# Optimization experiments

Hardware: AMD Instinct MI355X
Metric: run time of the kernel (lower is better)

## Reference

```python
import jax, jax.numpy as jnp
import numpy as np

SPATIAL_SHAPES = [(128, 128), (64, 64), (32, 32), (16, 16)]  # (H_l, W_l) per level
NUM_HEADS = 8
NUM_LEVELS = 4
NUM_POINTS = 4
EMBED_DIM = 256
HEAD_DIM = EMBED_DIM // NUM_HEADS
LEN_V = sum(h * w for h, w in SPATIAL_SHAPES)  # 21760
BS, LQ = 8, 900


def setup_inputs() -> dict:
    key = jax.random.key(0)
    ks = jax.random.split(key, 12)
    s = 0.05
    return {
        'query': jax.random.normal(ks[0], (BS, LQ, EMBED_DIM), jnp.float32),
        'reference_points': jax.random.uniform(ks[1], (BS, LQ, NUM_LEVELS, 2), jnp.float32),
        'value': jax.random.normal(ks[2], (BS, LEN_V, EMBED_DIM), jnp.float32),
        'w_value': jax.random.normal(ks[3], (EMBED_DIM, EMBED_DIM), jnp.float32) * s,
        'b_value': jnp.zeros((EMBED_DIM,), jnp.float32),
        'w_off': jax.random.normal(ks[4], (EMBED_DIM, NUM_HEADS * NUM_LEVELS * NUM_POINTS * 2), jnp.float32) * s,
        'b_off': jax.random.normal(ks[5], (NUM_HEADS * NUM_LEVELS * NUM_POINTS * 2,), jnp.float32),
        'w_attn': jax.random.normal(ks[6], (EMBED_DIM, NUM_HEADS * NUM_LEVELS * NUM_POINTS), jnp.float32) * s,
        'b_attn': jnp.zeros((NUM_HEADS * NUM_LEVELS * NUM_POINTS,), jnp.float32),
        'w_out': jax.random.normal(ks[7], (EMBED_DIM, EMBED_DIM), jnp.float32) * s,
        'b_out': jnp.zeros((EMBED_DIM,), jnp.float32),
    }


def _bilinear_sample(val, locx, locy, H, W):
    # val: [bs, nh, H*W, hd]; locx/locy: [bs, nh, N] normalized in [0,1]
    # grid_sample semantics: align_corners=False, zero padding.
    px = locx * W - 0.5
    py = locy * H - 0.5
    x0 = jnp.floor(px)
    y0 = jnp.floor(py)
    dx = px - x0
    dy = py - y0
    x0i = x0.astype(jnp.int32)
    y0i = y0.astype(jnp.int32)
    out = jnp.zeros(val.shape[:2] + (locx.shape[-1], val.shape[-1]), val.dtype)
    corners = [
        (x0i, y0i, (1 - dx) * (1 - dy)),
        (x0i + 1, y0i, dx * (1 - dy)),
        (x0i, y0i + 1, (1 - dx) * dy),
        (x0i + 1, y0i + 1, dx * dy),
    ]
    for xi, yi, w in corners:
        valid = ((xi >= 0) & (xi < W) & (yi >= 0) & (yi < H)).astype(val.dtype)
        idx = jnp.clip(yi, 0, H - 1) * W + jnp.clip(xi, 0, W - 1)
        g = jnp.take_along_axis(val, idx[..., None], axis=2)  # [bs,nh,N,hd]
        out = out + g * (w * valid)[..., None]
    return out


def reference(query, reference_points, value, w_value, b_value, w_off, b_off,
              w_attn, b_attn, w_out, b_out):
    bs, Lq, C = query.shape
    # value projection -> [bs, Lv, nh, hd]
    v = (value @ w_value + b_value).reshape(bs, -1, NUM_HEADS, HEAD_DIM)
    # sampling offsets [bs,Lq,nh,L,P,2], attention weights softmax over L*P
    off = (query @ w_off + b_off).reshape(bs, Lq, NUM_HEADS, NUM_LEVELS, NUM_POINTS, 2)
    aw = (query @ w_attn + b_attn).reshape(bs, Lq, NUM_HEADS, NUM_LEVELS * NUM_POINTS)
    aw = jax.nn.softmax(aw, axis=-1).reshape(bs, Lq, NUM_HEADS, NUM_LEVELS, NUM_POINTS)
    # normalizer is (W_l, H_l) per level (flip of spatial shapes)
    norm = jnp.asarray([[w, h] for h, w in SPATIAL_SHAPES], query.dtype)  # [L,2]
    loc = reference_points[:, :, None, :, None, :] + off / norm[None, None, None, :, None, :]
    # per-level bilinear sampling and weighted reduction
    out = jnp.zeros((bs, Lq, NUM_HEADS, HEAD_DIM), query.dtype)
    start = 0
    for l, (H, W) in enumerate(SPATIAL_SHAPES):
        vl = v[:, start:start + H * W]                       # [bs,HW,nh,hd]
        vl = vl.transpose(0, 2, 1, 3)                        # [bs,nh,HW,hd]
        ll = loc[:, :, :, l].transpose(0, 2, 1, 3, 4)        # [bs,nh,Lq,P,2]
        ll = ll.reshape(bs, NUM_HEADS, Lq * NUM_POINTS, 2)
        s = _bilinear_sample(vl, ll[..., 0], ll[..., 1], H, W)
        s = s.reshape(bs, NUM_HEADS, Lq, NUM_POINTS, HEAD_DIM)
        out = out + jnp.einsum('bhqpd,bqhp->bqhd', s, aw[:, :, :, l])
        start += H * W
    out = out.reshape(bs, Lq, C)
    return out @ w_out + b_out
```

## Files before the change

kernel.cpp:

```cpp
#include <hip/hip_runtime.h>

#define BS 8
#define LQ 900
#define NH 8
#define NL 4
#define NP 4
#define HD 32
#define ED 256
#define LEN_V 21760

typedef __attribute__((ext_vector_type(8))) short bf16x8;
typedef __attribute__((ext_vector_type(4))) float f32x4;
typedef __attribute__((ext_vector_type(4))) float fv4;

static __device__ __forceinline__ unsigned short f2bf(float f) {
  union { float f; unsigned u; } x; x.f = f;
  unsigned r = x.u + 0x7fffu + ((x.u >> 16) & 1u);
  return (unsigned short)(r >> 16);
}
static __device__ __forceinline__ float bf2f(unsigned short s) {
  union { unsigned u; float f; } x; x.u = ((unsigned)s) << 16;
  return x.f;
}
static __device__ __forceinline__ unsigned pack2(float a, float b) {
  return (unsigned)f2bf(a) | ((unsigned)f2bf(b) << 16);
}

__global__ __launch_bounds__(256, 3) void vproj_kernel(
    const float* __restrict__ value, const float* __restrict__ w,
    const float* __restrict__ bias, unsigned short* __restrict__ vout) {
  const int t = threadIdx.x;
  const int row0 = blockIdx.x * 64;
  const int wv = t >> 6;
  const int lane = t & 63;
  const int quad = lane >> 4;
  const int nn = lane & 15;

  __shared__ unsigned short a_lds[4 * 64 * 8];
  __shared__ unsigned short b_lds[4 * 256 * 8];

  f32x4 acc[4][4];
#pragma unroll
  for (int i = 0; i < 4; i++)
#pragma unroll
    for (int j = 0; j < 4; j++) acc[i][j] = (f32x4)(0.f);

  const int arow = t >> 2;
  const int akseg = t & 3;
  const int bkseg = wv;
  const int bn = lane;

  for (int k0 = 0; k0 < 256; k0 += 32) {
    __syncthreads();
    {
      const float* pa = &value[(row0 + arow) * 256 + k0 + akseg * 8];
      fv4 v0 = __builtin_nontemporal_load((const fv4*)pa);
      fv4 v1 = __builtin_nontemporal_load((const fv4*)(pa + 4));
      uint4 pk;
      pk.x = pack2(v0.x, v0.y);
      pk.y = pack2(v0.z, v0.w);
      pk.z = pack2(v1.x, v1.y);
      pk.w = pack2(v1.z, v1.w);
      *(uint4*)&a_lds[(akseg * 64 + arow) * 8] = pk;
    }
    {
      const float* pb = &w[(k0 + bkseg * 8) * 256 + bn];
#pragma unroll
      for (int c = 0; c < 4; c++) {
        float f[8];
#pragma unroll
        for (int j = 0; j < 8; j++) f[j] = pb[j * 256 + c * 64];
        uint4 pk;
        pk.x = pack2(f[0], f[1]);
        pk.y = pack2(f[2], f[3]);
        pk.z = pack2(f[4], f[5]);
        pk.w = pack2(f[6], f[7]);
        *(uint4*)&b_lds[(bkseg * 256 + c * 64 + bn) * 8] = pk;
      }
    }
    __syncthreads();

    bf16x8 af[4], bf[4];
#pragma unroll
    for (int rt = 0; rt < 4; rt++)
      af[rt] = *(const bf16x8*)&a_lds[(quad * 64 + rt * 16 + nn) * 8];
#pragma unroll
    for (int ct = 0; ct < 4; ct++)
      bf[ct] = *(const bf16x8*)&b_lds[(quad * 256 + wv * 64 + ct * 16 + nn) * 8];
#pragma unroll
    for (int rt = 0; rt < 4; rt++)
#pragma unroll
      for (int ct = 0; ct < 4; ct++)
        acc[rt][ct] = __builtin_amdgcn_mfma_f32_16x16x32_bf16(
            af[rt], bf[ct], acc[rt][ct], 0, 0, 0);
  }

#pragma unroll
  for (int ct = 0; ct < 4; ct++) {
    const int col = wv * 64 + ct * 16 + nn;
    const float bv = bias[col];
    const int h = col >> 5;
    const int d = col & 31;
#pragma unroll
    for (int rt = 0; rt < 4; rt++) {
      f32x4 f = acc[rt][ct];
#pragma unroll
      for (int reg = 0; reg < 4; reg++) {
        const int grow = row0 + rt * 16 + quad * 4 + reg;
        const int b = grow / LEN_V;
        const int s = grow - b * LEN_V;
        vout[((b * NH + h) * LEN_V + s) * HD + d] = f2bf(f[reg] + bv);
      }
    }
  }
}

__global__ __launch_bounds__(384, 2) void offattn_kernel(
    const float* __restrict__ query,
    const float* __restrict__ w_off, const float* __restrict__ b_off,
    const float* __restrict__ w_attn, const float* __restrict__ b_attn,
    float* __restrict__ OFF, float* __restrict__ LOG) {
  const int t = threadIdx.x;
  const int row0 = blockIdx.x * 32;
  const int rg = t / 96;
  const int c4 = t % 96;
  const int col = c4 * 4;
  const bool isOff = col < 256;
  const float* wbase = isOff ? (w_off + col) : (w_attn + (col - 256));
  const int wstride = isOff ? 256 : 128;
  const float* bb = isOff ? (b_off + col) : (b_attn + (col - 256));
  __shared__ float a_lds[32][8];

  float4 acc[8];
#pragma unroll
  for (int r = 0; r < 8; r++) acc[r] = make_float4(0.f, 0.f, 0.f, 0.f);

  for (int k0 = 0; k0 < 256; k0 += 8) {
    __syncthreads();
    if (t < 256) a_lds[t >> 3][t & 7] = query[(row0 + (t >> 3)) * 256 + k0 + (t & 7)];
    __syncthreads();
    float4 wr[8];
#pragma unroll
    for (int k = 0; k < 8; k++)
      wr[k] = *(const float4*)&wbase[(k0 + k) * wstride];
#pragma unroll
    for (int r = 0; r < 8; r++) {
      const float* ar = &a_lds[rg * 8 + r][0];
      float4 a0 = *(const float4*)&ar[0];
      float4 a1 = *(const float4*)&ar[4];
      float4 s = acc[r];
      s.x += a0.x*wr[0].x + a0.y*wr[1].x + a0.z*wr[2].x + a0.w*wr[3].x
           + a1.x*wr[4].x + a1.y*wr[5].x + a1.z*wr[6].x + a1.w*wr[7].x;
      s.y += a0.x*wr[0].y + a0.y*wr[1].y + a0.z*wr[2].y + a0.w*wr[3].y
           + a1.x*wr[4].y + a1.y*wr[5].y + a1.z*wr[6].y + a1.w*wr[7].y;
      s.z += a0.x*wr[0].z + a0.y*wr[1].z + a0.z*wr[2].z + a0.w*wr[3].z
           + a1.x*wr[4].z + a1.y*wr[5].z + a1.z*wr[6].z + a1.w*wr[7].z;
      s.w += a0.x*wr[0].w + a0.y*wr[1].w + a0.z*wr[2].w + a0.w*wr[3].w
           + a1.x*wr[4].w + a1.y*wr[5].w + a1.z*wr[6].w + a1.w*wr[7].w;
      acc[r] = s;
    }
  }

  const float4 bv = *(const float4*)bb;
#pragma unroll
  for (int r = 0; r < 8; r++) {
    const int grow = row0 + rg * 8 + r;
    float4 o = make_float4(acc[r].x + bv.x, acc[r].y + bv.y,
                           acc[r].z + bv.z, acc[r].w + bv.w);
    if (isOff) *(float4*)&OFF[grow * 256 + col] = o;
    else       *(float4*)&LOG[grow * 128 + (col - 256)] = o;
  }
}

__global__ __launch_bounds__(256, 4) void sample_kernel(
    const float* __restrict__ refp, const unsigned short* __restrict__ vp,
    const float* __restrict__ OFF, const float* __restrict__ LOG,
    float* __restrict__ RES) {
  const int t = threadIdx.x;
  const int b = blockIdx.x / (LQ / 4);
  const int q0 = (blockIdx.x % (LQ / 4)) * 4;

  __shared__ float off_lds[4][256];
  __shared__ float aw_lds[4][128];
  __shared__ float ref_lds[4][4][2];
  __shared__ int   soff[512][4];
  __shared__ float swt[512][4];

#pragma unroll
  for (int qi = 0; qi < 4; qi++)
    off_lds[qi][t] = OFF[(b * LQ + q0 + qi) * 256 + t];
  if (t < 128) {
#pragma unroll
    for (int qi = 0; qi < 4; qi++)
      aw_lds[qi][t] = LOG[(b * LQ + q0 + qi) * 128 + t];
  }
  if (t < 32) {
    const int qi = t >> 3, l = (t >> 1) & 3, xy = t & 1;
    ref_lds[qi][l][xy] = refp[((b * LQ + q0 + qi) * NL + l) * 2 + xy];
  }
  __syncthreads();

  if (t < 32) {
    const int qi = t >> 3, h = t & 7;
    float* a = &aw_lds[qi][h * 16];
    float m = a[0];
#pragma unroll
    for (int i = 1; i < 16; i++) m = fmaxf(m, a[i]);
    float e[16];
    float ssum = 0.f;
#pragma unroll
    for (int i = 0; i < 16; i++) { e[i] = __expf(a[i] - m); ssum += e[i]; }
    const float inv = 1.f / ssum;
#pragma unroll
    for (int i = 0; i < 16; i++) a[i] = e[i] * inv;
  }
  __syncthreads();

#pragma unroll
  for (int ss = 0; ss < 2; ss++) {
    const int sid = t + ss * 256;
    const int p = sid & 3, l = (sid >> 2) & 3, h = (sid >> 4) & 7, qi = sid >> 7;
    const int W = 128 >> l;
    const int base = (l == 0) ? 0 : ((l == 1) ? 16384 : ((l == 2) ? 20480 : 21504));
    const float Wf = (float)W;
    const float refx = ref_lds[qi][l][0];
    const float refy = ref_lds[qi][l][1];
    const float offx = off_lds[qi][h * 32 + l * 8 + p * 2 + 0];
    const float offy = off_lds[qi][h * 32 + l * 8 + p * 2 + 1];
    const float aw = aw_lds[qi][h * 16 + l * 4 + p];
    const float px = refx * Wf + offx - 0.5f;
    const float py = refy * Wf + offy - 0.5f;
    const float x0f = floorf(px), y0f = floorf(py);
    const float dx = px - x0f, dy = py - y0f;
    const int x0 = (int)x0f, y0 = (int)y0f;
    const int x1 = x0 + 1, y1 = y0 + 1;
    const float mx0 = (x0 >= 0 && x0 < W) ? 1.f : 0.f;
    const float mx1 = (x1 >= 0 && x1 < W) ? 1.f : 0.f;
    const float my0 = (y0 >= 0 && y0 < W) ? 1.f : 0.f;
    const float my1 = (y1 >= 0 && y1 < W) ? 1.f : 0.f;
    const int x0c = min(max(x0, 0), W - 1);
    const int x1c = min(max(x1, 0), W - 1);
    const int y0c = min(max(y0, 0), W - 1);
    const int y1c = min(max(y1, 0), W - 1);
    soff[sid][0] = (base + y0c * W + x0c) * 16;
    soff[sid][1] = (base + y0c * W + x1c) * 16;
    soff[sid][2] = (base + y1c * W + x0c) * 16;
    soff[sid][3] = (base + y1c * W + x1c) * 16;
    swt[sid][0] = (1.f - dx) * (1.f - dy) * mx0 * my0 * aw;
    swt[sid][1] = dx * (1.f - dy) * mx1 * my0 * aw;
    swt[sid][2] = (1.f - dx) * dy * mx0 * my1 * aw;
    swt[sid][3] = dx * dy * mx1 * my1 * aw;
  }
  __syncthreads();

  const int qsel = t >> 7;
  const int hh = (t >> 4) & 7;
  const int d2 = t & 15;
  const unsigned* vpu = (const unsigned*)vp + (size_t)(b * NH + hh) * (LEN_V * HD / 2);
#pragma unroll
  for (int j = 0; j < 2; j++) {
    const int qi = qsel * 2 + j;
    float r0 = 0.f, r1 = 0.f;
#pragma unroll
    for (int lp = 0; lp < 16; lp++) {
      const int sid = ((qi * 8 + hh) << 4) + lp;
      const int4 o = *(const int4*)&soff[sid][0];
      const float4 w = *(const float4*)&swt[sid][0];
      const unsigned u00 = vpu[o.x + d2];
      const unsigned u10 = vpu[o.y + d2];
      const unsigned u01 = vpu[o.z + d2];
      const unsigned u11 = vpu[o.w + d2];
      r0 += w.x * bf2f((unsigned short)(u00 & 0xffff))
          + w.y * bf2f((unsigned short)(u10 & 0xffff))
          + w.z * bf2f((unsigned short)(u01 & 0xffff))
          + w.w * bf2f((unsigned short)(u11 & 0xffff));
      r1 += w.x * bf2f((unsigned short)(u00 >> 16))
          + w.y * bf2f((unsigned short)(u10 >> 16))
          + w.z * bf2f((unsigned short)(u01 >> 16))
          + w.w * bf2f((unsigned short)(u11 >> 16));
    }
    float2 rr = make_float2(r0, r1);
    *(float2*)&RES[(b * LQ + q0 + qi) * 256 + hh * 32 + d2 * 2] = rr;
  }
}

__global__ __launch_bounds__(256, 2) void outproj_kernel(
    const float* __restrict__ RES, const float* __restrict__ w,
    const float* __restrict__ bias, float* __restrict__ out) {
  const int t = threadIdx.x;
  const int row0 = blockIdx.x * 32;
  const int rg = t >> 6;
  const int c0 = (t & 63) << 2;
  __shared__ float a_lds[32][8];

  float4 acc[8];
#pragma unroll
  for (int r = 0; r < 8; r++) acc[r] = make_float4(0.f, 0.f, 0.f, 0.f);

  const int lr = t >> 3;
  const int lk = t & 7;
  for (int k0 = 0; k0 < 256; k0 += 8) {
    __syncthreads();
    a_lds[lr][lk] = RES[(row0 + lr) * 256 + k0 + lk];
    __syncthreads();
    float4 wr[8];
#pragma unroll
    for (int k = 0; k < 8; k++)
      wr[k] = *(const float4*)&w[(k0 + k) * 256 + c0];
#pragma unroll
    for (int r = 0; r < 8; r++) {
      const float* ar = &a_lds[rg * 8 + r][0];
      float4 a0 = *(const float4*)&ar[0];
      float4 a1 = *(const float4*)&ar[4];
      float4 s = acc[r];
      s.x += a0.x*wr[0].x + a0.y*wr[1].x + a0.z*wr[2].x + a0.w*wr[3].x
           + a1.x*wr[4].x + a1.y*wr[5].x + a1.z*wr[6].x + a1.w*wr[7].x;
      s.y += a0.x*wr[0].y + a0.y*wr[1].y + a0.z*wr[2].y + a0.w*wr[3].y
           + a1.x*wr[4].y + a1.y*wr[5].y + a1.z*wr[6].y + a1.w*wr[7].y;
      s.z += a0.x*wr[0].z + a0.y*wr[1].z + a0.z*wr[2].z + a0.w*wr[3].z
           + a1.x*wr[4].z + a1.y*wr[5].z + a1.z*wr[6].z + a1.w*wr[7].z;
      s.w += a0.x*wr[0].w + a0.y*wr[1].w + a0.z*wr[2].w + a0.w*wr[3].w
           + a1.x*wr[4].w + a1.y*wr[5].w + a1.z*wr[6].w + a1.w*wr[7].w;
      acc[r] = s;
    }
  }

  const float4 bv = *(const float4*)&bias[c0];
#pragma unroll
  for (int r = 0; r < 8; r++) {
    const int grow = row0 + rg * 8 + r;
    float4 o = make_float4(acc[r].x + bv.x, acc[r].y + bv.y,
                           acc[r].z + bv.z, acc[r].w + bv.w);
    *(float4*)&out[grow * 256 + c0] = o;
  }
}

extern "C" void kernel_launch(void* const* d_in, const int* in_sizes, int n_in,
                              void* d_out, int out_size, void* d_ws, size_t ws_size,
                              hipStream_t stream) {
  (void)in_sizes; (void)n_in; (void)out_size; (void)ws_size;
  const float* query   = (const float*)d_in[0];
  const float* refp    = (const float*)d_in[1];
  const float* value   = (const float*)d_in[2];
  const float* w_value = (const float*)d_in[3];
  const float* b_value = (const float*)d_in[4];
  const float* w_off   = (const float*)d_in[5];
  const float* b_off   = (const float*)d_in[6];
  const float* w_attn  = (const float*)d_in[7];
  const float* b_attn  = (const float*)d_in[8];
  const float* w_out   = (const float*)d_in[9];
  const float* b_out   = (const float*)d_in[10];
  float* out = (float*)d_out;

  char* ws = (char*)d_ws;
  unsigned short* vp = (unsigned short*)ws;
  float* OFF = (float*)(ws + 89128960);
  float* LOG = (float*)(ws + 89128960 + 7372800);
  float* RES = (float*)(ws + 89128960 + 7372800 + 3686400);

  vproj_kernel<<<(BS * LEN_V) / 64, 256, 0, stream>>>(value, w_value, b_value, vp);
  offattn_kernel<<<(BS * LQ) / 32, 384, 0, stream>>>(query, w_off, b_off,
                                                     w_attn, b_attn, OFF, LOG);
  sample_kernel<<<BS * (LQ / 4), 256, 0, stream>>>(refp, vp, OFF, LOG, RES);
  outproj_kernel<<<(BS * LQ) / 32, 256, 0, stream>>>(RES, w_out, b_out, out);
}
```

Baseline: 443.1 us.

## Pre-convert value weights to bf16 and load MFMA fragments directly from global

Adds a small prep kernel that converts w_value to bf16 once, in the MFMA-swizzled layout. The value-projection GEMM then drops its LDS staging and barriers: each wave loads its A fragments straight from global memory and converts them in registers, and reads B fragments from the pre-packed buffer. This removes the repeated per-block fp32 weight conversion and the shared-memory round trips. In exchange, the A rows are loaded redundantly by each of the four waves and the launch count grows by one.

```diff
diff --git a/kernel.cpp b/kernel.cpp
--- a/kernel.cpp
+++ b/kernel.cpp
@@ -25,9 +25,35 @@
 static __device__ __forceinline__ unsigned pack2(float a, float b) {
   return (unsigned)f2bf(a) | ((unsigned)f2bf(b) << 16);
 }
+static __device__ __forceinline__ bf16x8 pack8(fv4 a, fv4 b) {
+  union { uint4 u; bf16x8 h; } x;
+  x.u.x = pack2(a.x, a.y);
+  x.u.y = pack2(a.z, a.w);
+  x.u.z = pack2(b.x, b.y);
+  x.u.w = pack2(b.z, b.w);
+  return x.h;
+}
+
+__global__ __launch_bounds__(256) void bprep_kernel(
+    const float* __restrict__ w, unsigned short* __restrict__ Bsw) {
+  const int id = blockIdx.x * 256 + threadIdx.x;
+  const int n = id & 255;
+  const int kseg = (id >> 8) & 3;
+  const int kc = id >> 10;
+  const float* src = &w[(kc * 32 + kseg * 8) * 256 + n];
+  float f[8];
+#pragma unroll
+  for (int j = 0; j < 8; j++) f[j] = src[j * 256];
+  uint4 pk;
+  pk.x = pack2(f[0], f[1]);
+  pk.y = pack2(f[2], f[3]);
+  pk.z = pack2(f[4], f[5]);
+  pk.w = pack2(f[6], f[7]);
+  *(uint4*)&Bsw[((kc * 4 + kseg) * 256 + n) * 8] = pk;
+}
 
 __global__ __launch_bounds__(256, 3) void vproj_kernel(
-    const float* __restrict__ value, const float* __restrict__ w,
+    const float* __restrict__ value, const unsigned short* __restrict__ Bsw,
     const float* __restrict__ bias, unsigned short* __restrict__ vout) {
   const int t = threadIdx.x;
   const int row0 = blockIdx.x * 64;
@@ -36,63 +62,34 @@
   const int quad = lane >> 4;
   const int nn = lane & 15;
 
-  __shared__ unsigned short a_lds[4 * 64 * 8];
-  __shared__ unsigned short b_lds[4 * 256 * 8];
-
   f32x4 acc[4][4];
 #pragma unroll
   for (int i = 0; i < 4; i++)
 #pragma unroll
     for (int j = 0; j < 4; j++) acc[i][j] = (f32x4)(0.f);
 
-  const int arow = t >> 2;
-  const int akseg = t & 3;
-  const int bkseg = wv;
-  const int bn = lane;
-
-  for (int k0 = 0; k0 < 256; k0 += 32) {
-    __syncthreads();
-    {
-      const float* pa = &value[(row0 + arow) * 256 + k0 + akseg * 8];
-      fv4 v0 = __builtin_nontemporal_load((const fv4*)pa);
-      fv4 v1 = __builtin_nontemporal_load((const fv4*)(pa + 4));
-      uint4 pk;
-      pk.x = pack2(v0.x, v0.y);
-      pk.y = pack2(v0.z, v0.w);
-      pk.z = pack2(v1.x, v1.y);
-      pk.w = pack2(v1.z, v1.w);
-      *(uint4*)&a_lds[(akseg * 64 + arow) * 8] = pk;
-    }
-    {
-      const float* pb = &w[(k0 + bkseg * 8) * 256 + bn];
-#pragma unroll
-      for (int c = 0; c < 4; c++) {
-        float f[8];
-#pragma unroll
-        for (int j = 0; j < 8; j++) f[j] = pb[j * 256 + c * 64];
-        uint4 pk;
-        pk.x = pack2(f[0], f[1]);
-        pk.y = pack2(f[2], f[3]);
-        pk.z = pack2(f[4], f[5]);
-        pk.w = pack2(f[6], f[7]);
-        *(uint4*)&b_lds[(bkseg * 256 + c * 64 + bn) * 8] = pk;
-      }
-    }
-    __syncthreads();
-
-    bf16x8 af[4], bf[4];
-#pragma unroll
-    for (int rt = 0; rt < 4; rt++)
-      af[rt] = *(const bf16x8*)&a_lds[(quad * 64 + rt * 16 + nn) * 8];
+  const float* aptr = &value[(row0 + nn) * 256 + quad * 8];
+  const unsigned short* bptr = &Bsw[(quad * 256 + wv * 64 + nn) * 8];
+
+#pragma unroll
+  for (int kc = 0; kc < 8; kc++) {
+    bf16x8 af[4], bfr[4];
+#pragma unroll
+    for (int rt = 0; rt < 4; rt++) {
+      const float* pa = aptr + rt * 16 * 256 + kc * 32;
+      fv4 v0 = *(const fv4*)pa;
+      fv4 v1 = *(const fv4*)(pa + 4);
+      af[rt] = pack8(v0, v1);
+    }
 #pragma unroll
     for (int ct = 0; ct < 4; ct++)
-      bf[ct] = *(const bf16x8*)&b_lds[(quad * 256 + wv * 64 + ct * 16 + nn) * 8];
+      bfr[ct] = *(const bf16x8*)(bptr + (kc * 1024 + ct * 16) * 8);
 #pragma unroll
     for (int rt = 0; rt < 4; rt++)
 #pragma unroll
       for (int ct = 0; ct < 4; ct++)
         acc[rt][ct] = __builtin_amdgcn_mfma_f32_16x16x32_bf16(
-            af[rt], bf[ct], acc[rt][ct], 0, 0, 0);
+            af[rt], bfr[ct], acc[rt][ct], 0, 0, 0);
   }
 
 #pragma unroll
@@ -357,8 +354,10 @@
   float* OFF = (float*)(ws + 89128960);
   float* LOG = (float*)(ws + 89128960 + 7372800);
   float* RES = (float*)(ws + 89128960 + 7372800 + 3686400);
-
-  vproj_kernel<<<(BS * LEN_V) / 64, 256, 0, stream>>>(value, w_value, b_value, vp);
+  unsigned short* Bsw = (unsigned short*)(ws + 89128960 + 7372800 + 3686400 + 7372800);
+
+  bprep_kernel<<<32, 256, 0, stream>>>(w_value, Bsw);
+  vproj_kernel<<<(BS * LEN_V) / 64, 256, 0, stream>>>(value, Bsw, b_value, vp);
   offattn_kernel<<<(BS * LQ) / 32, 384, 0, stream>>>(query, w_off, b_off,
                                                      w_attn, b_attn, OFF, LOG);
   sample_kernel<<<BS * (LQ / 4), 256, 0, stream>>>(refp, vp, OFF, LOG, RES);
```

Measured after the change: 483.2 us. 1.09x slower.
